# Performance work log

Hardware: AMD Instinct MI355X
Metric: run time of the kernel (lower is better)

Reference implementation:

```python
import jax, jax.numpy as jnp
import numpy as np

TAU = 0.1                 # gumbel-softmax temperature used in forward
LAMBDA_SMOOTH = 0.1       # default lambda_smooth
HALF_LOG_2PI = 0.9189385332046727
NUM_STATES = 3


def setup_inputs() -> dict:
    key = jax.random.key(0)
    k_x, k_e, k_g = jax.random.split(key, 3)
    S, B, E = 2048, 3000, 12288  # spots, genomic bins, spatial edges
    x = jax.random.normal(k_x, (S, B), dtype=jnp.float32)
    # concatenation of per-chromosome [start,end) bin ranges covering all bins
    bin_idx = jnp.arange(B, dtype=jnp.int32)
    edge_index = jax.random.randint(k_e, (2, E), 0, S, dtype=jnp.int32)
    # matches torch's  -log(Exponential(1))  = Gumbel(0,1) noise
    gumbel_noise = jax.random.gumbel(k_g, (S, B, NUM_STATES), dtype=jnp.float32)
    state_means = jnp.array([-1.0, 1.0], dtype=jnp.float32)
    log_stds = jnp.array([-1.0, -1.0, -1.0], dtype=jnp.float32)
    return dict(x=x, bin_idx=bin_idx, edge_index=edge_index,
                gumbel_noise=gumbel_noise, state_means=state_means,
                log_stds=log_stds)


def _forward(x, gumbel_noise, state_means, log_stds, bin_idx, edge_index):
    # all_means = [mean_loss, 0, mean_gain]
    all_means = jnp.stack([state_means[0], jnp.zeros((), x.dtype), state_means[1]])
    stds = jnp.exp(log_stds) + 1e-6                       # [3]
    z = (x[..., None] - all_means) / stds                 # [S, B, 3]
    log_em = -0.5 * z * z - jnp.log(stds) - HALF_LOG_2PI  # Normal log_prob
    # per-chromosome slicing + concat == one gather over covered bins
    log_em = jnp.take(log_em, bin_idx, axis=1)            # [S, Bc, 3]
    gnoise = jnp.take(gumbel_noise, bin_idx, axis=1)      # [S, Bc, 3]
    logits = (log_em + gnoise) / TAU
    y_soft = jax.nn.softmax(logits, axis=-1)
    y_hard = jax.nn.one_hot(jnp.argmax(y_soft, axis=-1), NUM_STATES, dtype=x.dtype)
    # straight-through hard one-hot
    states = y_hard - jax.lax.stop_gradient(y_soft) + y_soft  # [S, Bc, 3]
    norm_copy = states @ all_means                            # [S, Bc]
    row, col = edge_index[0], edge_index[1]
    diff = states[row] - states[col]                          # [E, Bc, 3]
    smooth_loss = LAMBDA_SMOOTH * jnp.mean(diff * diff)
    return norm_copy, smooth_loss


def reference(x, bin_idx, edge_index, gumbel_noise, state_means, log_stds):
    return _forward(x, gumbel_noise, state_means, log_stds, bin_idx, edge_index)
```

## Files before the change

### kernel.cpp

```cpp
#include <hip/hip_runtime.h>
#include <math.h>

#define S_SPOTS 2048
#define B_BINS 3000
#define E_EDGES 12288
#define SB_TOTAL (S_SPOTS * B_BINS)
#define SB4 (SB_TOTAL / 4)
#define ROW_BYTES 768
#define ROW_DW 192
#define ST_BYTES (S_SPOTS * ROW_BYTES)


__global__ __launch_bounds__(256) void map_kernel(
        const float4* __restrict__ x4,
        const float4* __restrict__ g4,
        const float* __restrict__ state_means,
        const float* __restrict__ log_stds,
        float4* __restrict__ out4,
        unsigned char* __restrict__ st) {
    __shared__ float4 lg[768];
    __shared__ double sp[6];
    int tid = threadIdx.x;
    int blk = blockIdx.x;

    if (tid == 0) {
        const double CHALF = 0.9189385332046727;
        for (int k = 0; k < 3; ++k) {
            double sd = exp((double)log_stds[k]) + 1e-6;
            sp[k]     = 1.0 / sd;
            sp[3 + k] = -log(sd) - CHALF;
        }
    }
    const float4* gg = g4 + (size_t)blk * 768;
    float4 t0 = gg[tid];
    float4 t1 = gg[tid + 256];
    float4 t2 = gg[tid + 512];
    int gi = blk * 256 + tid;
    float4 xv = x4[gi];
    float m0f = state_means[0];
    float m2f = state_means[1];
    lg[tid] = t0; lg[tid + 256] = t1; lg[tid + 512] = t2;
    __syncthreads();

    double r0 = sp[0], r1 = sp[1], r2 = sp[2];
    double cc0 = sp[3], cc1 = sp[4], cc2 = sp[5];
    double m0 = (double)m0f, m2 = (double)m2f;

    const float4* myg = (const float4*)((const char*)lg + 48 * tid);
    float4 ga = myg[0], gb = myg[1], gc = myg[2];
    float xs[4]  = {xv.x, xv.y, xv.z, xv.w};
    float gs[12] = {ga.x, ga.y, ga.z, ga.w, gb.x, gb.y, gb.z, gb.w,
                    gc.x, gc.y, gc.z, gc.w};
    float os[4];
    unsigned pk = 0;
#pragma unroll
    for (int j = 0; j < 4; ++j) {
        double x = (double)xs[j];
        double z0 = (x - m0) * r0;
        double z1 = x * r1;
        double z2 = (x - m2) * r2;
        double l0 = fma(-0.5 * z0, z0, cc0) + (double)gs[3 * j + 0];
        double l1 = fma(-0.5 * z1, z1, cc1) + (double)gs[3 * j + 1];
        double l2 = fma(-0.5 * z2, z2, cc2) + (double)gs[3 * j + 2];
        int k = 0; double best = l0;
        if (l1 > best) { best = l1; k = 1; }
        if (l2 > best) { best = l2; k = 2; }
        os[j] = (k == 0) ? m0f : ((k == 1) ? 0.0f : m2f);
        pk |= (unsigned)k << (2 * j);
    }
    out4[gi] = make_float4(os[0], os[1], os[2], os[3]);
    unsigned sb0  = 4u * (unsigned)gi;
    unsigned row  = sb0 / 3000u;
    unsigned colb = (sb0 % 3000u) >> 2;
    st[row * ROW_BYTES + colb] = (unsigned char)pk;
}

__global__ __launch_bounds__(256) void edge_kernel(
        const int* __restrict__ edge_index,
        const unsigned int* __restrict__ st,
        unsigned int* __restrict__ counter,
        unsigned int* __restrict__ done,
        float* __restrict__ out) {
    int lane = threadIdx.x & 63;
    int wid  = threadIdx.x >> 6;
    int gw   = blockIdx.x * 4 + wid;
    unsigned cnt = 0;
#pragma unroll
    for (int t = 0; t < 3; ++t) {
        int e = gw * 3 + t;
        int r = edge_index[e];
        int c = edge_index[E_EDGES + e];
        const unsigned* pr = st + r * ROW_DW;
        const unsigned* pc = st + c * ROW_DW;
        unsigned a0 = pr[lane], a1 = pr[lane + 64], a2 = pr[lane + 128];
        unsigned b0 = pc[lane], b1 = pc[lane + 64], b2 = pc[lane + 128];
        unsigned v0 = a0 ^ b0, v1 = a1 ^ b1, v2 = a2 ^ b2;
        cnt += (unsigned)__popc((v0 | (v0 >> 1)) & 0x55555555u);
        cnt += (unsigned)__popc((v1 | (v1 >> 1)) & 0x55555555u);
        cnt += (unsigned)__popc((v2 | (v2 >> 1)) & 0x55555555u);
    }
    for (int off = 32; off; off >>= 1)
        cnt += __shfl_down(cnt, off, 64);
    __shared__ unsigned wsum[4];
    if (lane == 0) wsum[wid] = cnt;
    __syncthreads();
    if (threadIdx.x == 0) {
        unsigned bs = wsum[0] + wsum[1] + wsum[2] + wsum[3];
        atomicAdd(counter, bs);
        __threadfence();
        unsigned old = atomicAdd(done, 1u);
        if (old == gridDim.x - 1) {
            __threadfence();
            unsigned total = atomicAdd(counter, 0u);
            double sum  = 2.0 * (double)total;
            double mean = sum / ((double)E_EDGES * (double)B_BINS * 3.0);
            out[SB_TOTAL] = (float)(0.1 * mean);
        }
    }
}

extern "C" void kernel_launch(void* const* d_in, const int* in_sizes, int n_in,
                              void* d_out, int out_size, void* d_ws, size_t ws_size,
                              hipStream_t stream) {
    const float* x           = (const float*)d_in[0];
    const int*   edge_index  = (const int*)d_in[2];
    const float* gumbel      = (const float*)d_in[3];
    const float* state_means = (const float*)d_in[4];
    const float* log_stds    = (const float*)d_in[5];
    float* out = (float*)d_out;

    unsigned char* st      = (unsigned char*)d_ws;
    unsigned int*  counter = (unsigned int*)((char*)d_ws + ST_BYTES);
    unsigned int*  done    = counter + 1;

    hipMemsetAsync(d_ws, 0, ST_BYTES + 8, stream);

    map_kernel<<<SB4 / 256, 256, 0, stream>>>(
        (const float4*)x, (const float4*)gumbel, state_means, log_stds,
        (float4*)d_out, st);
    edge_kernel<<<E_EDGES / 12, 256, 0, stream>>>(
        edge_index, (const unsigned int*)st, counter, done, out);
}
```

Before: 171.6 us.

## Drop workspace memset, spread edge-count atomics across padded slots

Removes the per-call memset of the whole state buffer. Padding bytes are never read now, because the last dword is masked and lanes past 60 are skipped, and the map kernel zeroes the counters. The edge kernel now uses one wave per edge with 512-thread blocks. Block partial sums go to 64 cache-line-padded atomic slots to reduce contention on one counter. The risks are that slot zeroing in block 0 relies on kernel ordering, and that unwritten workspace padding must truly never be read.

Measured after the change: 186.5 us. 8.7% more time.

```diff
diff --git a/kernel.cpp b/kernel.cpp
--- a/kernel.cpp
+++ b/kernel.cpp
@@ -9,6 +9,7 @@
 #define ROW_BYTES 768
 #define ROW_DW 192
 #define ST_BYTES (S_SPOTS * ROW_BYTES)
+#define NSLOT 64
 
 
 __global__ __launch_bounds__(256) void map_kernel(
@@ -17,12 +18,14 @@
         const float* __restrict__ state_means,
         const float* __restrict__ log_stds,
         float4* __restrict__ out4,
-        unsigned char* __restrict__ st) {
+        unsigned char* __restrict__ st,
+        unsigned int* __restrict__ slots) {
     __shared__ float4 lg[768];
     __shared__ double sp[6];
     int tid = threadIdx.x;
     int blk = blockIdx.x;
 
+    if (blk == 0 && tid <= NSLOT) slots[tid * 16] = 0u;
     if (tid == 0) {
         const double CHALF = 0.9189385332046727;
         for (int k = 0; k < 3; ++k) {
@@ -75,43 +78,44 @@
     st[row * ROW_BYTES + colb] = (unsigned char)pk;
 }
 
-__global__ __launch_bounds__(256) void edge_kernel(
+__global__ __launch_bounds__(512) void edge_kernel(
         const int* __restrict__ edge_index,
         const unsigned int* __restrict__ st,
-        unsigned int* __restrict__ counter,
-        unsigned int* __restrict__ done,
+        unsigned int* __restrict__ slots,
         float* __restrict__ out) {
     int lane = threadIdx.x & 63;
     int wid  = threadIdx.x >> 6;
-    int gw   = blockIdx.x * 4 + wid;
-    unsigned cnt = 0;
-#pragma unroll
-    for (int t = 0; t < 3; ++t) {
-        int e = gw * 3 + t;
-        int r = edge_index[e];
-        int c = edge_index[E_EDGES + e];
-        const unsigned* pr = st + r * ROW_DW;
-        const unsigned* pc = st + c * ROW_DW;
-        unsigned a0 = pr[lane], a1 = pr[lane + 64], a2 = pr[lane + 128];
-        unsigned b0 = pc[lane], b1 = pc[lane + 64], b2 = pc[lane + 128];
-        unsigned v0 = a0 ^ b0, v1 = a1 ^ b1, v2 = a2 ^ b2;
-        cnt += (unsigned)__popc((v0 | (v0 >> 1)) & 0x55555555u);
-        cnt += (unsigned)__popc((v1 | (v1 >> 1)) & 0x55555555u);
-        cnt += (unsigned)__popc((v2 | (v2 >> 1)) & 0x55555555u);
-    }
+    int e    = blockIdx.x * 8 + wid;
+    int r = edge_index[e];
+    int c = edge_index[E_EDGES + e];
+    const unsigned* pr = st + r * ROW_DW;
+    const unsigned* pc = st + c * ROW_DW;
+    unsigned a0 = pr[lane], b0 = pc[lane];
+    unsigned a1 = pr[lane + 64], b1 = pc[lane + 64];
+    unsigned a2 = 0, b2 = 0;
+    if (lane < 60) { a2 = pr[lane + 128]; b2 = pc[lane + 128]; }
+    unsigned v0 = a0 ^ b0, v1 = a1 ^ b1, v2 = a2 ^ b2;
+    if (lane == 59) v2 &= 0x0000FFFFu;
+    unsigned cnt = (unsigned)__popc((v0 | (v0 >> 1)) & 0x55555555u)
+                 + (unsigned)__popc((v1 | (v1 >> 1)) & 0x55555555u)
+                 + (unsigned)__popc((v2 | (v2 >> 1)) & 0x55555555u);
     for (int off = 32; off; off >>= 1)
         cnt += __shfl_down(cnt, off, 64);
-    __shared__ unsigned wsum[4];
+    __shared__ unsigned wsum[8];
     if (lane == 0) wsum[wid] = cnt;
     __syncthreads();
     if (threadIdx.x == 0) {
-        unsigned bs = wsum[0] + wsum[1] + wsum[2] + wsum[3];
-        atomicAdd(counter, bs);
+        unsigned bs = 0;
+#pragma unroll
+        for (int w = 0; w < 8; ++w) bs += wsum[w];
+        atomicAdd(&slots[(blockIdx.x & (NSLOT - 1)) * 16], bs);
         __threadfence();
-        unsigned old = atomicAdd(done, 1u);
+        unsigned old = atomicAdd(&slots[NSLOT * 16], 1u);
         if (old == gridDim.x - 1) {
             __threadfence();
-            unsigned total = atomicAdd(counter, 0u);
+            unsigned total = 0;
+            for (int s = 0; s < NSLOT; ++s)
+                total += atomicAdd(&slots[s * 16], 0u);
             double sum  = 2.0 * (double)total;
             double mean = sum / ((double)E_EDGES * (double)B_BINS * 3.0);
             out[SB_TOTAL] = (float)(0.1 * mean);
@@ -129,15 +133,12 @@
     const float* log_stds    = (const float*)d_in[5];
     float* out = (float*)d_out;
 
-    unsigned char* st      = (unsigned char*)d_ws;
-    unsigned int*  counter = (unsigned int*)((char*)d_ws + ST_BYTES);
-    unsigned int*  done    = counter + 1;
-
-    hipMemsetAsync(d_ws, 0, ST_BYTES + 8, stream);
+    unsigned char* st    = (unsigned char*)d_ws;
+    unsigned int*  slots = (unsigned int*)((char*)d_ws + ST_BYTES);
 
     map_kernel<<<SB4 / 256, 256, 0, stream>>>(
         (const float4*)x, (const float4*)gumbel, state_means, log_stds,
-        (float4*)d_out, st);
-    edge_kernel<<<E_EDGES / 12, 256, 0, stream>>>(
-        edge_index, (const unsigned int*)st, counter, done, out);
+        (float4*)d_out, st, slots);
+    edge_kernel<<<E_EDGES / 8, 512, 0, stream>>>(
+        edge_index, (const unsigned int*)st, slots, out);
 }
```
